# Optimization experiments

Hardware: AMD Instinct MI355X
Metric: run time of the kernel (lower is better)

The kernel has to match this reference:

```python
import jax, jax.numpy as jnp
import numpy as np


def _pairwise_dist(e, c):
    # Euclidean distance matrix [N, K], matching torch.cdist(p=2)
    e2 = jnp.sum(e * e, axis=1, keepdims=True)          # [N, 1]
    c2 = jnp.sum(c * c, axis=1)[None, :]                # [1, K]
    d2 = e2 + c2 - 2.0 * (e @ c.T)                      # [N, K]
    return jnp.sqrt(jnp.maximum(d2, 0.0))


def setup_inputs() -> dict:
    key = jax.random.key(0)
    k1, k2 = jax.random.split(key)
    N, K, D = 262144, 1024, 128
    embeddings = jax.random.normal(k1, (N, D), dtype=jnp.float32)
    cluster_centroids = jax.random.normal(k2, (K, D), dtype=jnp.float32)
    return {"embeddings": embeddings, "cluster_centroids": cluster_centroids}


def reference(embeddings, cluster_centroids):
    dist = _pairwise_dist(embeddings, cluster_centroids)   # [N, K]
    labels = jnp.argmin(dist, axis=1)                      # [N]
    logits = -dist
    # CrossEntropyLoss(mean): logsumexp(logits) - logits[label]
    # logits[label] = -min(dist) since label is the argmin
    lse = jax.nn.logsumexp(logits, axis=1)                 # [N]
    target_logit = -jnp.min(dist, axis=1)                  # [N]
    loss = jnp.mean(lse - target_logit)
    return (loss, labels)
```

## Files before the change

### kernel.cpp

```cpp
#include <hip/hip_runtime.h>
#include <stdint.h>

#define D_DIM 128
#define K_DIM 1024
#define BM 64
#define N_TOTAL 262144
#define TAU 0.1f
#define MAXF 16384

typedef __attribute__((ext_vector_type(8))) short short8;
typedef __attribute__((ext_vector_type(4))) float f32x4;

__device__ __forceinline__ unsigned short f2bf(float f) {
    union { float f; uint32_t u; } v; v.f = f;
    uint32_t r = v.u + 0x7fffu + ((v.u >> 16) & 1u);
    return (unsigned short)(r >> 16);
}
__device__ __forceinline__ float bf2f(unsigned short h) {
    union { float f; uint32_t u; } v; v.u = ((uint32_t)h) << 16;
    return v.f;
}

__global__ void prep_c2_kernel(const float* __restrict__ C,
                               float* __restrict__ c2) {
    int col = blockIdx.x * blockDim.x + threadIdx.x;
    if (col >= K_DIM) return;
    const float4* C4 = (const float4*)(C + (size_t)col * D_DIM);
    float s0 = 0.f, s1 = 0.f, s2 = 0.f, s3 = 0.f;
    #pragma unroll
    for (int dq = 0; dq < 32; ++dq) {
        float4 v = C4[dq];
        s0 = fmaf(v.x, v.x, s0);
        s1 = fmaf(v.y, v.y, s1);
        s2 = fmaf(v.z, v.z, s2);
        s3 = fmaf(v.w, v.w, s3);
    }
    c2[col] = (s0 + s1) + (s2 + s3);
}

__global__ void prep_frag_kernel(const float* __restrict__ C,
                                 unsigned short* __restrict__ Cfrag) {
    int g = blockIdx.x * blockDim.x + threadIdx.x;
    int col = g >> 5;
    int dq = g & 31;
    float4 v = ((const float4*)C)[g];
    unsigned short h0 = f2bf(v.x), h1 = f2bf(v.y), h2 = f2bf(v.z), h3 = f2bf(v.w);
    unsigned short l0 = f2bf(v.x - bf2f(h0)), l1 = f2bf(v.y - bf2f(h1));
    unsigned short l2 = f2bf(v.z - bf2f(h2)), l3 = f2bf(v.w - bf2f(h3));
    int ntg = col >> 4;
    int cl = col & 15;
    int d0 = dq << 2;
    int ds = d0 >> 5;
    int lane = (((d0 >> 3) & 3) << 4) | cl;
    int jb = d0 & 7;
    size_t idx = (((size_t)(ntg * 4 + ds) * 64 + lane) * 8 + jb);
    uint2 hv = make_uint2((uint32_t)h0 | ((uint32_t)h1 << 16),
                          (uint32_t)h2 | ((uint32_t)h3 << 16));
    uint2 lv = make_uint2((uint32_t)l0 | ((uint32_t)l1 << 16),
                          (uint32_t)l2 | ((uint32_t)l3 << 16));
    *(uint2*)&Cfrag[idx] = hv;
    *(uint2*)&Cfrag[131072 + idx] = lv;
}

__global__ __launch_bounds__(256, 2) void fused_mfma_kernel(
        const float* __restrict__ E,
        const unsigned short* __restrict__ Cfrag,
        const float* __restrict__ c2g,
        float* __restrict__ out,
        int* __restrict__ fcnt,
        int* __restrict__ flist)
{
    __shared__ unsigned short Elds[32 * 528];
    __shared__ float c2s[K_DIM];
    __shared__ float e2s[BM];
    __shared__ uint32_t mrgk[BM * 2];
    __shared__ uint32_t mrgm[BM * 2];
    __shared__ float    mrgs[BM * 2];

    const int tid = threadIdx.x;
    const int lane = tid & 63;
    const int w = tid >> 6;
    const int Rh = w >> 1;
    const int Nh = w & 1;
    const int q = lane >> 4;
    const int mcol = lane & 15;
    const int row0 = blockIdx.x * BM;

    if (tid < BM) e2s[tid] = 0.f;
    for (int i = tid; i < K_DIM; i += 256) c2s[i] = c2g[i];
    __syncthreads();

    {
        const float4* E4 = (const float4*)(E + (size_t)row0 * D_DIM);
        #pragma unroll
        for (int it = 0; it < 8; ++it) {
            int chunk = it * 256 + tid;
            int r = chunk >> 5;
            int dq = chunk & 31;
            float4 v = E4[chunk];
            float p = fmaf(v.x, v.x, fmaf(v.y, v.y, fmaf(v.z, v.z, v.w * v.w)));
            atomicAdd(&e2s[r], p);
            unsigned short h0 = f2bf(v.x), h1 = f2bf(v.y), h2 = f2bf(v.z), h3 = f2bf(v.w);
            unsigned short l0 = f2bf(v.x - bf2f(h0)), l1 = f2bf(v.y - bf2f(h1));
            unsigned short l2 = f2bf(v.z - bf2f(h2)), l3 = f2bf(v.w - bf2f(h3));
            int d0 = dq << 2;
            int mt = r >> 4;
            int ds = d0 >> 5;
            int lane_slot = (((d0 >> 3) & 3) << 4) | (r & 15);
            int jb = d0 & 7;
            int segh = (mt * 4 + ds) * 528 + lane_slot * 8 + jb;
            uint2 hv = make_uint2((uint32_t)h0 | ((uint32_t)h1 << 16),
                                  (uint32_t)h2 | ((uint32_t)h3 << 16));
            uint2 lv = make_uint2((uint32_t)l0 | ((uint32_t)l1 << 16),
                                  (uint32_t)l2 | ((uint32_t)l3 << 16));
            *(uint2*)&Elds[segh] = hv;
            *(uint2*)&Elds[16 * 528 + segh] = lv;
        }
    }
    __syncthreads();

    float e2r[8];
    #pragma unroll
    for (int s = 0; s < 8; ++s)
        e2r[s] = e2s[(Rh * 2 + (s >> 2)) * 16 + q * 4 + (s & 3)];

    uint32_t k1v[8], m2v[8];
    float sv[8];
    #pragma unroll
    for (int s = 0; s < 8; ++s) { k1v[s] = 0xFFFFFFFFu; m2v[s] = 0xFFFFFFFFu; sv[s] = 0.f; }

    const short8* Bfrag = (const short8*)Cfrag;

    #pragma unroll 1
    for (int kc = 0; kc < 8; ++kc) {
        f32x4 acc[2][4];
        #pragma unroll
        for (int i = 0; i < 2; ++i)
            #pragma unroll
            for (int j = 0; j < 4; ++j)
                acc[i][j] = (f32x4){0.f, 0.f, 0.f, 0.f};

        #pragma unroll
        for (int ds = 0; ds < 4; ++ds) {
            short8 ah[2], al[2];
            #pragma unroll
            for (int mi = 0; mi < 2; ++mi) {
                int seg = ((Rh * 2 + mi) * 4 + ds) * 528 + lane * 8;
                ah[mi] = *(const short8*)&Elds[seg];
                al[mi] = *(const short8*)&Elds[16 * 528 + seg];
            }
            #pragma unroll
            for (int ni = 0; ni < 4; ++ni) {
                int ntg = kc * 8 + Nh * 4 + ni;
                size_t bidx = ((size_t)ntg * 4 + ds) * 64 + lane;
                short8 bh = Bfrag[bidx];
                short8 bl = Bfrag[16384 + bidx];
                #pragma unroll
                for (int mi = 0; mi < 2; ++mi) {
                    acc[mi][ni] = __builtin_amdgcn_mfma_f32_16x16x32_bf16(al[mi], bh, acc[mi][ni], 0, 0, 0);
                    acc[mi][ni] = __builtin_amdgcn_mfma_f32_16x16x32_bf16(ah[mi], bl, acc[mi][ni], 0, 0, 0);
                    acc[mi][ni] = __builtin_amdgcn_mfma_f32_16x16x32_bf16(ah[mi], bh, acc[mi][ni], 0, 0, 0);
                }
            }
        }
        #pragma unroll
        for (int ni = 0; ni < 4; ++ni) {
            int kidx = kc * 128 + Nh * 64 + ni * 16 + mcol;
            float c2v = c2s[kidx];
            #pragma unroll
            for (int mi = 0; mi < 2; ++mi) {
                #pragma unroll
                for (int r = 0; r < 4; ++r) {
                    int s = mi * 4 + r;
                    float d2 = fmaf(-2.f, acc[mi][ni][r], e2r[s] + c2v);
                    d2 = fmaxf(d2, 0.f);
                    uint32_t key = (__float_as_uint(d2) & 0xFFFFFC00u) | (uint32_t)kidx;
                    float dist = __builtin_amdgcn_sqrtf(d2);
                    sv[s] += __expf(-dist);
                    uint32_t k1 = k1v[s];
                    m2v[s] = min(m2v[s], max(k1, key));
                    k1v[s] = min(k1, key);
                }
            }
        }
    }

    #pragma unroll
    for (int s = 0; s < 8; ++s) {
        #pragma unroll
        for (int off = 1; off < 16; off <<= 1) {
            uint32_t ok1 = __shfl_xor(k1v[s], off);
            uint32_t om2 = __shfl_xor(m2v[s], off);
            float osv = __shfl_xor(sv[s], off);
            m2v[s] = min(min(m2v[s], om2), max(k1v[s], ok1));
            k1v[s] = min(k1v[s], ok1);
            sv[s] += osv;
        }
    }
    if (mcol == 0) {
        #pragma unroll
        for (int s = 0; s < 8; ++s) {
            int row = (Rh * 2 + (s >> 2)) * 16 + q * 4 + (s & 3);
            mrgk[row * 2 + Nh] = k1v[s];
            mrgm[row * 2 + Nh] = m2v[s];
            mrgs[row * 2 + Nh] = sv[s];
        }
    }
    __syncthreads();

    if (tid < BM) {
        uint32_t ka = mrgk[tid * 2 + 0], kb = mrgk[tid * 2 + 1];
        uint32_t ma = mrgm[tid * 2 + 0], mb = mrgm[tid * 2 + 1];
        float ss = mrgs[tid * 2 + 0] + mrgs[tid * 2 + 1];
        uint32_t k1 = min(ka, kb);
        uint32_t m2 = min(min(ma, mb), max(ka, kb));
        float m1q = __uint_as_float(k1 & 0xFFFFFC00u);
        float m2q = __uint_as_float(m2 & 0xFFFFFC00u);
        int i1 = (int)(k1 & 1023u);
        float lossr = logf(ss) + sqrtf(m1q);
        out[1 + row0 + tid] = (float)i1;
        if (m2q - m1q < TAU) {
            int idx = atomicAdd(fcnt, 1);
            if (idx < MAXF) flist[idx] = row0 + tid;
        }
        float v = lossr;
        #pragma unroll
        for (int off = 32; off > 0; off >>= 1) v += __shfl_down(v, off);
        if (tid == 0) atomicAdd(out, v * (1.0f / (float)N_TOTAL));
    }
}

__global__ void refine_kernel(const float* __restrict__ E,
                              const float* __restrict__ C,
                              const float* __restrict__ c2g,
                              const int* __restrict__ fcnt,
                              const int* __restrict__ flist,
                              float* __restrict__ out) {
    int cnt = *fcnt;
    if (cnt > MAXF) cnt = MAXF;
    int base = blockIdx.x * 4;
    if (base >= cnt) return;
    int nr = cnt - base;
    if (nr > 4) nr = 4;

    __shared__ float Er[4][D_DIM];
    __shared__ float e2r_[4];
    __shared__ float2 red[256];

    const int tid = threadIdx.x;
    int rows[4];
    #pragma unroll
    for (int r = 0; r < 4; ++r) {
        int rr = r < nr ? r : (nr - 1);
        rows[r] = flist[base + rr];
    }
    for (int i = tid; i < 4 * D_DIM; i += 256) {
        int rr = i >> 7;
        int dd = i & 127;
        Er[rr][dd] = E[(size_t)rows[rr] * D_DIM + dd];
    }
    __syncthreads();
    if (tid < 4) {
        float s = 0.f;
        for (int d = 0; d < D_DIM; ++d) s = fmaf(Er[tid][d], Er[tid][d], s);
        e2r_[tid] = s;
    }
    __syncthreads();

    float bm[4] = {1e30f, 1e30f, 1e30f, 1e30f};
    float bk[4] = {0.f, 0.f, 0.f, 0.f};
    for (int ii = 0; ii < 4; ++ii) {
        int k = ii * 256 + tid;
        float dot0 = 0.f, dot1 = 0.f, dot2 = 0.f, dot3 = 0.f;
        const float4* C4 = (const float4*)(C + (size_t)k * D_DIM);
        for (int dq = 0; dq < 32; ++dq) {
            float4 cv = C4[dq];
            int d0 = dq * 4;
            dot0 = fmaf(Er[0][d0], cv.x, fmaf(Er[0][d0 + 1], cv.y, fmaf(Er[0][d0 + 2], cv.z, fmaf(Er[0][d0 + 3], cv.w, dot0))));
            dot1 = fmaf(Er[1][d0], cv.x, fmaf(Er[1][d0 + 1], cv.y, fmaf(Er[1][d0 + 2], cv.z, fmaf(Er[1][d0 + 3], cv.w, dot1))));
            dot2 = fmaf(Er[2][d0], cv.x, fmaf(Er[2][d0 + 1], cv.y, fmaf(Er[2][d0 + 2], cv.z, fmaf(Er[2][d0 + 3], cv.w, dot2))));
            dot3 = fmaf(Er[3][d0], cv.x, fmaf(Er[3][d0 + 1], cv.y, fmaf(Er[3][d0 + 2], cv.z, fmaf(Er[3][d0 + 3], cv.w, dot3))));
        }
        float c2v = c2g[k];
        float dd[4];
        dd[0] = dot0; dd[1] = dot1; dd[2] = dot2; dd[3] = dot3;
        #pragma unroll
        for (int r = 0; r < 4; ++r) {
            float d2 = (e2r_[r] + c2v) - 2.f * dd[r];
            float dist = sqrtf(fmaxf(d2, 0.f));
            if (dist < bm[r]) { bm[r] = dist; bk[r] = (float)k; }
        }
    }
    for (int r = 0; r < nr; ++r) {
        red[tid] = make_float2(bm[r], bk[r]);
        __syncthreads();
        for (int off = 128; off > 0; off >>= 1) {
            if (tid < off) {
                float2 o = red[tid + off];
                float2 m = red[tid];
                if (o.x < m.x || (o.x == m.x && o.y < m.y)) red[tid] = o;
            }
            __syncthreads();
        }
        if (tid == 0) out[1 + rows[r]] = red[0].y;
        __syncthreads();
    }
}

extern "C" void kernel_launch(void* const* d_in, const int* in_sizes, int n_in,
                              void* d_out, int out_size, void* d_ws, size_t ws_size,
                              hipStream_t stream) {
    const float* E = (const float*)d_in[0];
    const float* C = (const float*)d_in[1];
    float* out = (float*)d_out;

    unsigned short* Cfrag = (unsigned short*)d_ws;
    float* c2 = (float*)((char*)d_ws + 524288);
    int* fcnt = (int*)((char*)d_ws + 524288 + 4096);
    int* flist = fcnt + 1;

    hipMemsetAsync(d_out, 0, sizeof(float), stream);
    hipMemsetAsync(fcnt, 0, sizeof(int), stream);

    prep_c2_kernel<<<dim3(16), dim3(64), 0, stream>>>(C, c2);
    prep_frag_kernel<<<dim3(128), dim3(256), 0, stream>>>(C, Cfrag);
    fused_mfma_kernel<<<dim3(N_TOTAL / BM), dim3(256), 0, stream>>>(E, Cfrag, c2, out, fcnt, flist);
    refine_kernel<<<dim3(MAXF / 4), dim3(256), 0, stream>>>(E, C, c2, fcnt, flist, out);
}
```

Measured before the change: 510.4 us.

## Fold sqrt/exp scaling into squared distances, use exp2, raise occupancy, rework refine

Pre-scales e2 and c2 by a constant sigma so the sqrt of the scaled distance feeds exp2 directly, replacing the __expf multiply, and fixes up the min-distance term with ln2 when the loss is computed. The clamp to zero becomes an fabs inside the sqrt, and the near-tie threshold is scaled to match. Per-row norms are now reduced with wave shuffles instead of LDS atomics, which also removes an initial barrier. Launch bounds go from 2 to 4 blocks per CU, which may force register spills. The refine kernel handles 8 rows per block and uses packed 64-bit keys with a shuffle-based argmin in place of the LDS tree with many barriers.

```diff
diff --git a/kernel.cpp b/kernel.cpp
--- a/kernel.cpp
+++ b/kernel.cpp
@@ -5,8 +5,19 @@
 #define K_DIM 1024
 #define BM 64
 #define N_TOTAL 262144
-#define TAU 0.1f
 #define MAXF 16384
+#define RR 8
+
+#define SIGMA 2.0813689810056077f
+#define NS2   (-2.0f * SIGMA)
+#define TAUS  (0.1f * SIGMA)
+#define LN2   0.69314718055994531f
+
+#if __has_builtin(__builtin_amdgcn_exp2f)
+#define EXP2F __builtin_amdgcn_exp2f
+#else
+#define EXP2F exp2f
+#endif
 
 typedef __attribute__((ext_vector_type(8))) short short8;
 typedef __attribute__((ext_vector_type(4))) float f32x4;
@@ -62,7 +73,7 @@
     *(uint2*)&Cfrag[131072 + idx] = lv;
 }
 
-__global__ __launch_bounds__(256, 2) void fused_mfma_kernel(
+__global__ __launch_bounds__(256, 4) void fused_mfma_kernel(
         const float* __restrict__ E,
         const unsigned short* __restrict__ Cfrag,
         const float* __restrict__ c2g,
@@ -86,20 +97,20 @@
     const int mcol = lane & 15;
     const int row0 = blockIdx.x * BM;
 
-    if (tid < BM) e2s[tid] = 0.f;
-    for (int i = tid; i < K_DIM; i += 256) c2s[i] = c2g[i];
-    __syncthreads();
+    for (int i = tid; i < K_DIM; i += 256) c2s[i] = SIGMA * c2g[i];
 
     {
         const float4* E4 = (const float4*)(E + (size_t)row0 * D_DIM);
-        #pragma unroll
+        #pragma unroll 4
         for (int it = 0; it < 8; ++it) {
             int chunk = it * 256 + tid;
             int r = chunk >> 5;
             int dq = chunk & 31;
             float4 v = E4[chunk];
             float p = fmaf(v.x, v.x, fmaf(v.y, v.y, fmaf(v.z, v.z, v.w * v.w)));
-            atomicAdd(&e2s[r], p);
+            #pragma unroll
+            for (int off = 1; off < 32; off <<= 1) p += __shfl_xor(p, off);
+            if ((tid & 31) == 0) e2s[r] = p;
             unsigned short h0 = f2bf(v.x), h1 = f2bf(v.y), h2 = f2bf(v.z), h3 = f2bf(v.w);
             unsigned short l0 = f2bf(v.x - bf2f(h0)), l1 = f2bf(v.y - bf2f(h1));
             unsigned short l2 = f2bf(v.z - bf2f(h2)), l3 = f2bf(v.w - bf2f(h3));
@@ -119,10 +130,10 @@
     }
     __syncthreads();
 
-    float e2r[8];
+    float e2rs[8];
     #pragma unroll
     for (int s = 0; s < 8; ++s)
-        e2r[s] = e2s[(Rh * 2 + (s >> 2)) * 16 + q * 4 + (s & 3)];
+        e2rs[s] = SIGMA * e2s[(Rh * 2 + (s >> 2)) * 16 + q * 4 + (s & 3)];
 
     uint32_t k1v[8], m2v[8];
     float sv[8];
@@ -172,11 +183,10 @@
                 #pragma unroll
                 for (int r = 0; r < 4; ++r) {
                     int s = mi * 4 + r;
-                    float d2 = fmaf(-2.f, acc[mi][ni][r], e2r[s] + c2v);
-                    d2 = fmaxf(d2, 0.f);
+                    float d2 = fmaf(NS2, acc[mi][ni][r], e2rs[s] + c2v);
                     uint32_t key = (__float_as_uint(d2) & 0xFFFFFC00u) | (uint32_t)kidx;
-                    float dist = __builtin_amdgcn_sqrtf(d2);
-                    sv[s] += __expf(-dist);
+                    float dist = __builtin_amdgcn_sqrtf(__builtin_fabsf(d2));
+                    sv[s] += EXP2F(-dist);
                     uint32_t k1 = k1v[s];
                     m2v[s] = min(m2v[s], max(k1, key));
                     k1v[s] = min(k1, key);
@@ -217,9 +227,9 @@
         float m1q = __uint_as_float(k1 & 0xFFFFFC00u);
         float m2q = __uint_as_float(m2 & 0xFFFFFC00u);
         int i1 = (int)(k1 & 1023u);
-        float lossr = logf(ss) + sqrtf(m1q);
+        float lossr = logf(ss) + sqrtf(m1q) * LN2;
         out[1 + row0 + tid] = (float)i1;
-        if (m2q - m1q < TAU) {
+        if (m2q - m1q < TAUS) {
             int idx = atomicAdd(fcnt, 1);
             if (idx < MAXF) flist[idx] = row0 + tid;
         }
@@ -238,72 +248,82 @@
                               float* __restrict__ out) {
     int cnt = *fcnt;
     if (cnt > MAXF) cnt = MAXF;
-    int base = blockIdx.x * 4;
+    int base = blockIdx.x * RR;
     if (base >= cnt) return;
-    int nr = cnt - base;
-    if (nr > 4) nr = 4;
-
-    __shared__ float Er[4][D_DIM];
-    __shared__ float e2r_[4];
-    __shared__ float2 red[256];
+
+    __shared__ float Er[RR][D_DIM];
+    __shared__ float e2r_[RR];
+    __shared__ int rowid[RR];
+    __shared__ unsigned long long wred[RR][4];
 
     const int tid = threadIdx.x;
-    int rows[4];
-    #pragma unroll
-    for (int r = 0; r < 4; ++r) {
-        int rr = r < nr ? r : (nr - 1);
-        rows[r] = flist[base + rr];
-    }
-    for (int i = tid; i < 4 * D_DIM; i += 256) {
-        int rr = i >> 7;
-        int dd = i & 127;
-        Er[rr][dd] = E[(size_t)rows[rr] * D_DIM + dd];
-    }
-    __syncthreads();
-    if (tid < 4) {
+    if (tid < RR) {
+        int rr = base + tid;
+        if (rr >= cnt) rr = cnt - 1;
+        rowid[tid] = flist[rr];
+    }
+    __syncthreads();
+    for (int i = tid; i < RR * 32; i += 256) {
+        int rr = i >> 5, dq = i & 31;
+        ((float4*)Er[rr])[dq] = ((const float4*)(E + (size_t)rowid[rr] * D_DIM))[dq];
+    }
+    __syncthreads();
+    if (tid < RR) {
         float s = 0.f;
         for (int d = 0; d < D_DIM; ++d) s = fmaf(Er[tid][d], Er[tid][d], s);
         e2r_[tid] = s;
     }
     __syncthreads();
 
-    float bm[4] = {1e30f, 1e30f, 1e30f, 1e30f};
-    float bk[4] = {0.f, 0.f, 0.f, 0.f};
+    unsigned long long best[RR];
+    #pragma unroll
+    for (int r = 0; r < RR; ++r) best[r] = ~0ull;
+
     for (int ii = 0; ii < 4; ++ii) {
         int k = ii * 256 + tid;
-        float dot0 = 0.f, dot1 = 0.f, dot2 = 0.f, dot3 = 0.f;
         const float4* C4 = (const float4*)(C + (size_t)k * D_DIM);
+        float dot[RR];
+        #pragma unroll
+        for (int r = 0; r < RR; ++r) dot[r] = 0.f;
         for (int dq = 0; dq < 32; ++dq) {
             float4 cv = C4[dq];
             int d0 = dq * 4;
-            dot0 = fmaf(Er[0][d0], cv.x, fmaf(Er[0][d0 + 1], cv.y, fmaf(Er[0][d0 + 2], cv.z, fmaf(Er[0][d0 + 3], cv.w, dot0))));
-            dot1 = fmaf(Er[1][d0], cv.x, fmaf(Er[1][d0 + 1], cv.y, fmaf(Er[1][d0 + 2], cv.z, fmaf(Er[1][d0 + 3], cv.w, dot1))));
-            dot2 = fmaf(Er[2][d0], cv.x, fmaf(Er[2][d0 + 1], cv.y, fmaf(Er[2][d0 + 2], cv.z, fmaf(Er[2][d0 + 3], cv.w, dot2))));
-            dot3 = fmaf(Er[3][d0], cv.x, fmaf(Er[3][d0 + 1], cv.y, fmaf(Er[3][d0 + 2], cv.z, fmaf(Er[3][d0 + 3], cv.w, dot3))));
+            #pragma unroll
+            for (int r = 0; r < RR; ++r) {
+                dot[r] = fmaf(Er[r][d0], cv.x,
+                          fmaf(Er[r][d0 + 1], cv.y,
+                           fmaf(Er[r][d0 + 2], cv.z,
+                            fmaf(Er[r][d0 + 3], cv.w, dot[r]))));
+            }
         }
         float c2v = c2g[k];
-        float dd[4];
-        dd[0] = dot0; dd[1] = dot1; dd[2] = dot2; dd[3] = dot3;
-        #pragma unroll
-        for (int r = 0; r < 4; ++r) {
-            float d2 = (e2r_[r] + c2v) - 2.f * dd[r];
+        #pragma unroll
+        for (int r = 0; r < RR; ++r) {
+            float d2 = (e2r_[r] + c2v) - 2.f * dot[r];
             float dist = sqrtf(fmaxf(d2, 0.f));
-            if (dist < bm[r]) { bm[r] = dist; bk[r] = (float)k; }
-        }
-    }
-    for (int r = 0; r < nr; ++r) {
-        red[tid] = make_float2(bm[r], bk[r]);
-        __syncthreads();
-        for (int off = 128; off > 0; off >>= 1) {
-            if (tid < off) {
-                float2 o = red[tid + off];
-                float2 m = red[tid];
-                if (o.x < m.x || (o.x == m.x && o.y < m.y)) red[tid] = o;
-            }
-            __syncthreads();
-        }
-        if (tid == 0) out[1 + rows[r]] = red[0].y;
-        __syncthreads();
+            unsigned long long key =
+                (((unsigned long long)__float_as_uint(dist)) << 10) | (unsigned)k;
+            best[r] = best[r] < key ? best[r] : key;
+        }
+    }
+
+    const int wv = tid >> 6;
+    #pragma unroll
+    for (int r = 0; r < RR; ++r) {
+        unsigned long long b = best[r];
+        #pragma unroll
+        for (int off = 32; off > 0; off >>= 1) {
+            unsigned long long o = __shfl_xor(b, off);
+            b = o < b ? o : b;
+        }
+        if ((tid & 63) == 0) wred[r][wv] = b;
+    }
+    __syncthreads();
+    if (tid < RR) {
+        unsigned long long b = wred[tid][0];
+        #pragma unroll
+        for (int j = 1; j < 4; ++j) b = wred[tid][j] < b ? wred[tid][j] : b;
+        out[1 + rowid[tid]] = (float)(int)(b & 1023u);
     }
 }
 
@@ -325,5 +345,5 @@
     prep_c2_kernel<<<dim3(16), dim3(64), 0, stream>>>(C, c2);
     prep_frag_kernel<<<dim3(128), dim3(256), 0, stream>>>(C, Cfrag);
     fused_mfma_kernel<<<dim3(N_TOTAL / BM), dim3(256), 0, stream>>>(E, Cfrag, c2, out, fcnt, flist);
-    refine_kernel<<<dim3(MAXF / 4), dim3(256), 0, stream>>>(E, C, c2, fcnt, flist, out);
-}
+    refine_kernel<<<dim3(MAXF / RR), dim3(256), 0, stream>>>(E, C, c2, fcnt, flist, out);
+}
```

New measurement: 789.7 us. 1.55x slower.
